# Optimization experiments

Measured on AMD Instinct MI355X. Metric: run time of the kernel, lower is better.

The kernel has to match this reference:

```python
import jax, jax.numpy as jnp
import numpy as np

B, T, N_EMBD = 1, 2048, 2048
N_HEAD = 16
KV_LOW = 512      # kv_low_rank == head_size (compressed value dim)
Q_LOW = 1024
ROPE_HS = 64
QK_HS = KV_LOW + ROPE_HS  # 576
HEAD_SIZE = KV_LOW        # v_equiv = c_kv.view(B,1,T,head_size)


def _rope_tables(seq_len, dim, base=10000.0):
    # litgpt-style: theta over half dim, duplicated to full dim
    inv = 1.0 / (base ** (np.arange(0, dim, 2, dtype=np.float32) / dim))
    t = np.arange(seq_len, dtype=np.float32)
    freqs = np.outer(t, inv)                      # [T, dim/2]
    emb = np.concatenate([freqs, freqs], axis=-1)  # [T, dim]
    return jnp.asarray(np.cos(emb)), jnp.asarray(np.sin(emb))


def _apply_rope(x, cos, sin):
    # x: [..., T, d]; cos/sin broadcastable [T, d]. rotate-half RoPE.
    d = x.shape[-1]
    x1, x2 = x[..., : d // 2], x[..., d // 2:]
    rotated = jnp.concatenate([-x2, x1], axis=-1)
    return x * cos + rotated * sin


def setup_inputs() -> dict:
    key = jax.random.key(0)
    ks = jax.random.split(key, 4)
    x = jax.random.normal(ks[0], (B, T, N_EMBD), dtype=jnp.float32)
    cos, sin = _rope_tables(T, ROPE_HS)
    s = 0.02
    W_qkv = jax.random.normal(ks[1], (N_EMBD, KV_LOW + ROPE_HS + Q_LOW), dtype=jnp.float32) * s
    W_qdec = jax.random.normal(ks[2], (Q_LOW, N_HEAD * QK_HS), dtype=jnp.float32) * s
    W_out = jax.random.normal(ks[3], (N_HEAD * HEAD_SIZE, N_EMBD), dtype=jnp.float32) * s
    return {"x": x, "cos": cos, "sin": sin, "W_qkv": W_qkv, "W_qdec": W_qdec, "W_out": W_out}


def reference(x, cos, sin, W_qkv, W_qdec, W_out):
    Bq, Tq, _ = x.shape
    # latent encoding and split
    latents = x @ W_qkv                                       # [B,T,kv+rope+q]
    c_kv = latents[..., :KV_LOW]                              # [B,T,512] (keys-nope and values)
    k_r = latents[..., KV_LOW:KV_LOW + ROPE_HS]               # [B,T,64]
    c_q = latents[..., KV_LOW + ROPE_HS:]                     # [B,T,1024]
    # per-head query decode
    q = (c_q @ W_qdec).reshape(Bq, Tq, N_HEAD, QK_HS)         # [B,T,H,576]
    q_nope, q_r = q[..., :KV_LOW], q[..., KV_LOW:]
    # partial RoPE
    k_r = _apply_rope(k_r, cos, sin)                          # [B,T,64]
    q_r = _apply_rope(q_r, cos[None, :, None, :], sin[None, :, None, :])  # [B,T,H,64]
    q = jnp.concatenate([q_nope, q_r], axis=-1)               # [B,T,H,576]
    q = jnp.swapaxes(q, 1, 2)                                 # [B,H,T,576]
    k = jnp.concatenate([c_kv, k_r], axis=-1)                 # [B,T,576] shared across heads
    v = c_kv                                                  # [B,T,512] shared across heads
    scale = 1.0 / jnp.sqrt(jnp.float32(HEAD_SIZE))
    scores = jnp.einsum('bhtd,bsd->bhts', q, k) * scale       # [B,H,T,T]
    causal = jnp.tril(jnp.ones((Tq, Tq), dtype=bool))
    scores = jnp.where(causal, scores, jnp.finfo(scores.dtype).min)
    attn = jax.nn.softmax(scores, axis=-1)
    y = jnp.einsum('bhts,bsd->bhtd', attn, v)                 # [B,H,T,512]
    y = jnp.swapaxes(y, 1, 2).reshape(Bq, Tq, N_HEAD * HEAD_SIZE)
    return y @ W_out                                          # [B,T,n_embd]
```

## Files before the change

kernel.cpp:

```cpp
#include <hip/hip_runtime.h>

typedef __bf16 bf16x8_t __attribute__((ext_vector_type(8)));
typedef float f32x4_t __attribute__((ext_vector_type(4)));

#define LAT_LD 1664
#define QK_DIM 576
#define V_DIM 512
#define NHEAD 16
#define TSEQ 2048
#define QLD 9216
#define YLD 8192
#define KLD 576
#define SCALE 0.044194173824159216f

__device__ __forceinline__ unsigned short f2bf(float f) {
  union { float f; unsigned int u; } v; v.f = f;
  unsigned int r = v.u + 0x7FFFu + ((v.u >> 16) & 1u);
  return (unsigned short)(r >> 16);
}

__device__ __forceinline__ void load_lds16(const unsigned short* g, unsigned short* l) {
  __builtin_amdgcn_global_load_lds((const __attribute__((address_space(1))) void*)g,
                                   (__attribute__((address_space(3))) void*)l, 16, 0, 0);
}

__device__ __forceinline__ void conv_t_body(const float* __restrict__ src, int R, int Csrc,
                                            unsigned short* __restrict__ dst,
                                            int bx, int by, int tid,
                                            unsigned short (*T)[72]) {
  const int r0 = bx * 64, c0 = by * 64;
  const bool live = (c0 < Csrc);
#pragma unroll
  for (int it = 0; it < 4; ++it) {
    int idx = it * 256 + tid;
    int r = idx >> 4, c4 = (idx & 15) * 4;
    float4 v = {0.f, 0.f, 0.f, 0.f};
    if (live) v = *(const float4*)&src[(size_t)(r0 + r) * Csrc + c0 + c4];
    T[c4 + 0][r] = f2bf(v.x);
    T[c4 + 1][r] = f2bf(v.y);
    T[c4 + 2][r] = f2bf(v.z);
    T[c4 + 3][r] = f2bf(v.w);
  }
  __syncthreads();
#pragma unroll
  for (int it = 0; it < 2; ++it) {
    int idx = it * 256 + tid;
    int cc = idx >> 3, r8 = (idx & 7) * 8;
    uint4 v = *(const uint4*)&T[cc][r8];
    *(uint4*)&dst[(size_t)(c0 + cc) * R + r0 + r8] = v;
  }
}

__global__ __launch_bounds__(256) void prep_all(
    const float* __restrict__ x, unsigned short* __restrict__ xb,
    const float* __restrict__ wqkv, unsigned short* __restrict__ wqkvT,
    const float* __restrict__ wqdec, unsigned short* __restrict__ wqdecT,
    const float* __restrict__ wout, unsigned short* __restrict__ woutT,
    float* __restrict__ lsum) {
  __shared__ unsigned short T[64][72];
  const int blk = blockIdx.x, tid = threadIdx.x;
  if (blk < 4096) {
    int i = (blk * 256 + tid) * 4;
    float4 v = *(const float4*)&x[i];
    ushort4 o;
    o.x = f2bf(v.x); o.y = f2bf(v.y); o.z = f2bf(v.z); o.w = f2bf(v.w);
    *(ushort4*)&xb[i] = o;
  } else if (blk < 4928) {
    int l = blk - 4096;
    conv_t_body(wqkv, 2048, 1600, wqkvT, l & 31, l >> 5, tid, T);
  } else if (blk < 7232) {
    int l = blk - 4928;
    conv_t_body(wqdec, 1024, 9216, wqdecT, l & 15, l >> 4, tid, T);
  } else if (blk < 11328) {
    int l = blk - 7232;
    conv_t_body(wout, 8192, 2048, woutT, l & 127, l >> 7, tid, T);
  } else {
    int i = ((blk - 11328) * 256 + tid) * 4;
    *(float4*)&lsum[i] = (float4){0.f, 0.f, 0.f, 0.f};
  }
}

__global__ __launch_bounds__(256) void postlat(
    const float* __restrict__ P1,
    unsigned short* __restrict__ lat,
    unsigned short* __restrict__ kbuf,
    unsigned short* __restrict__ vtg,
    const float* __restrict__ cosb, const float* __restrict__ sinb) {
  __shared__ unsigned short T[64][72];
  const int tid = threadIdx.x;
  const int bx = blockIdx.x, by = blockIdx.y;
  const int r0 = bx * 64, c0 = by * 64;
  const size_t n = (size_t)2048 * 1664;

#pragma unroll
  for (int it = 0; it < 4; ++it) {
    int idx = it * 256 + tid;
    int r = idx >> 4, c4 = (idx & 15) * 4;
    size_t off = (size_t)(r0 + r) * 1664 + c0 + c4;
    float4 a = *(const float4*)&P1[off];
    float4 b = *(const float4*)&P1[n + off];
    ushort4 o;
    o.x = f2bf(a.x + b.x); o.y = f2bf(a.y + b.y);
    o.z = f2bf(a.z + b.z); o.w = f2bf(a.w + b.w);
    if (by < 8) {
      *(ushort4*)&kbuf[(size_t)(r0 + r) * KLD + c0 + c4] = o;
      T[c4 + 0][r] = o.x; T[c4 + 1][r] = o.y; T[c4 + 2][r] = o.z; T[c4 + 3][r] = o.w;
    } else if (by == 8) {
      T[r][c4 + 0] = o.x; T[r][c4 + 1] = o.y; T[r][c4 + 2] = o.z; T[r][c4 + 3] = o.w;
    } else {
      *(ushort4*)&lat[(size_t)(r0 + r) * LAT_LD + c0 + c4] = o;
    }
  }
  if (by > 8) return;
  __syncthreads();
  if (by < 8) {
#pragma unroll
    for (int it = 0; it < 2; ++it) {
      int idx = it * 256 + tid;
      int cc = idx >> 3, r8 = (idx & 7) * 8;
      uint4 v = *(const uint4*)&T[cc][r8];
      *(uint4*)&vtg[(size_t)(c0 + cc) * TSEQ + r0 + r8] = v;
    }
  } else {
#pragma unroll
    for (int it = 0; it < 8; ++it) {
      int idx = it * 256 + tid;
      int r = idx >> 5, d = idx & 31;
      int t = r0 + r;
      union { unsigned int u; float f; } a, b;
      a.u = ((unsigned int)T[r][d]) << 16;
      b.u = ((unsigned int)T[r][d + 32]) << 16;
      float c0f = cosb[t * 64 + d], s0f = sinb[t * 64 + d];
      float c1f = cosb[t * 64 + d + 32], s1f = sinb[t * 64 + d + 32];
      kbuf[(size_t)t * KLD + 512 + d] = f2bf(a.f * c0f - b.f * s0f);
      kbuf[(size_t)t * KLD + 544 + d] = f2bf(b.f * c1f + a.f * s1f);
    }
  }
}

#define GEMM_PROLOGUE()                                                     \
  __shared__ __align__(16) unsigned short As[8192];                         \
  __shared__ __align__(16) unsigned short Bs[8192];                         \
  const int tid = threadIdx.x;                                              \
  const int wave = tid >> 6, lane = tid & 63;                               \
  const int quad = lane >> 4, l16 = lane & 15;                              \
  const int wm = wave >> 1, wn = wave & 1;                                  \
  f32x4_t acc[4][4];                                                        \
  f32x4_t zero = {0.f, 0.f, 0.f, 0.f};                                      \
  _Pragma("unroll") for (int mi = 0; mi < 4; ++mi)                          \
    _Pragma("unroll") for (int ni = 0; ni < 4; ++ni) acc[mi][ni] = zero;

#define GEMM_KLOOP(Aptr, Alda, Bptr, Bldb, M0, N0, KLEN)                    \
  for (int k0 = 0; k0 < (KLEN); k0 += 64) {                                 \
    _Pragma("unroll") for (int p2 = 0; p2 < 2; ++p2) {                      \
      int ci = p2 * 256 + tid;                                              \
      int rr2 = ci >> 2, cc2 = (ci & 3) * 8;                                \
      const unsigned short* ga = &(Aptr)[(size_t)((M0) + rr2) * (Alda) + k0 + cc2]; \
      const unsigned short* gb = &(Bptr)[(size_t)((N0) + rr2) * (Bldb) + k0 + cc2]; \
      load_lds16(ga,      &As[ci * 8]);                                     \
      load_lds16(ga + 32, &As[4096 + ci * 8]);                              \
      load_lds16(gb,      &Bs[ci * 8]);                                     \
      load_lds16(gb + 32, &Bs[4096 + ci * 8]);                              \
    }                                                                       \
    __syncthreads();                                                        \
    _Pragma("unroll") for (int hf = 0; hf < 2; ++hf) {                      \
      bf16x8_t af[4], bfr[4];                                               \
      _Pragma("unroll") for (int mi = 0; mi < 4; ++mi)                      \
        af[mi] = *(const bf16x8_t*)&As[hf * 4096 + (wm * 64 + mi * 16 + l16) * 32 + quad * 8]; \
      _Pragma("unroll") for (int ni = 0; ni < 4; ++ni)                      \
        bfr[ni] = *(const bf16x8_t*)&Bs[hf * 4096 + (wn * 64 + ni * 16 + l16) * 32 + quad * 8]; \
      _Pragma("unroll") for (int mi = 0; mi < 4; ++mi)                      \
        _Pragma("unroll") for (int ni = 0; ni < 4; ++ni)                    \
          acc[mi][ni] = __builtin_amdgcn_mfma_f32_16x16x32_bf16(af[mi], bfr[ni], acc[mi][ni], 0, 0, 0); \
    }                                                                       \
    __syncthreads();                                                        \
  }

__global__ __launch_bounds__(256, 2) void gemm_splitk(
    const unsigned short* __restrict__ A, int lda,
    const unsigned short* __restrict__ Bt, int ldb,
    float* __restrict__ P, int ldc, int Ks) {
  const int m0 = blockIdx.y * 128, n0 = blockIdx.x * 128;
  const size_t koff = (size_t)blockIdx.z * Ks;
  const unsigned short* Ap = A + koff;
  const unsigned short* Bp = Bt + koff;
  float* C = P + (size_t)blockIdx.z * ((size_t)gridDim.y * 128) * ldc;
  GEMM_PROLOGUE();
  GEMM_KLOOP(Ap, lda, Bp, ldb, m0, n0, Ks);
#pragma unroll
  for (int mi = 0; mi < 4; ++mi)
#pragma unroll
    for (int ni = 0; ni < 4; ++ni)
#pragma unroll
      for (int r = 0; r < 4; ++r) {
        int row = m0 + wm * 64 + mi * 16 + quad * 4 + r;
        int col = n0 + wn * 64 + ni * 16 + l16;
        C[(size_t)row * ldc + col] = acc[mi][ni][r];
      }
}

__global__ __launch_bounds__(256, 2) void gemm_qdec(
    const unsigned short* __restrict__ A,
    const unsigned short* __restrict__ Bt,
    unsigned short* __restrict__ qbuf,
    const float* __restrict__ cosb, const float* __restrict__ sinb) {
  const int m0 = blockIdx.y * 128, n0 = blockIdx.x * 128;
  GEMM_PROLOGUE();
  GEMM_KLOOP(A, LAT_LD, Bt, 1024, m0, n0, 1024);

  const int cb = n0 + wn * 64;
  const bool ropeh = (cb % QK_DIM) == 512;
#pragma unroll
  for (int mi = 0; mi < 4; ++mi)
#pragma unroll
    for (int r = 0; r < 4; ++r) {
      int t = m0 + wm * 64 + mi * 16 + quad * 4 + r;
      if (ropeh) {
#pragma unroll
        for (int ni = 0; ni < 2; ++ni) {
          int d = ni * 16 + l16;
          float c0f = cosb[t * 64 + d], s0f = sinb[t * 64 + d];
          float c1f = cosb[t * 64 + d + 32], s1f = sinb[t * 64 + d + 32];
          float v1 = acc[mi][ni][r], v2 = acc[mi][ni + 2][r];
          qbuf[(size_t)t * QLD + cb + d] = f2bf(v1 * c0f - v2 * s0f);
          qbuf[(size_t)t * QLD + cb + 32 + d] = f2bf(v2 * c1f + v1 * s1f);
        }
      } else {
#pragma unroll
        for (int ni = 0; ni < 4; ++ni)
          qbuf[(size_t)t * QLD + cb + ni * 16 + l16] = f2bf(acc[mi][ni][r]);
      }
    }
}

__global__ __launch_bounds__(256) void reduce4_f32(const float* __restrict__ p,
                                                   float* __restrict__ dst, int n) {
  int i = (blockIdx.x * 256 + threadIdx.x) * 4;
  if (i < n) {
    float4 a = *(const float4*)&p[i];
    float4 b = *(const float4*)&p[(size_t)n + i];
    float4 c = *(const float4*)&p[2 * (size_t)n + i];
    float4 d = *(const float4*)&p[3 * (size_t)n + i];
    float4 o;
    o.x = (a.x + b.x) + (c.x + d.x);
    o.y = (a.y + b.y) + (c.y + d.y);
    o.z = (a.z + b.z) + (c.z + d.z);
    o.w = (a.w + b.w) + (c.w + d.w);
    *(float4*)&dst[i] = o;
  }
}

__global__ __launch_bounds__(256, 2) void qke_kernel(
    const unsigned short* __restrict__ qbuf,
    const unsigned short* __restrict__ kbuf,
    unsigned short* __restrict__ Ebuf,
    float* __restrict__ lsum, int hbase) {
  int tx = blockIdx.x, ig = 15, cnt = 16;
  while (tx >= cnt) { tx -= cnt; --ig; --cnt; }
  const int j = tx;
  const int hl = blockIdx.y, h = hbase + hl;
  const int Kmax = (ig + 1) << 7;
  const int r0g = ig << 7;
  const int pre = (ig * (ig + 1)) >> 1;

  const unsigned short* A = qbuf + (size_t)r0g * QLD + h * QK_DIM;
  const unsigned short* Bt = kbuf + (size_t)(j << 7) * KLD;
  unsigned short* Eh = Ebuf + ((size_t)hl * 136 + pre) * 16384;

  GEMM_PROLOGUE();
  GEMM_KLOOP(A, QLD, Bt, KLD, 0, 0, QK_DIM);

#pragma unroll
  for (int mi = 0; mi < 4; ++mi) {
    float rs[4] = {0.f, 0.f, 0.f, 0.f};
#pragma unroll
    for (int ni = 0; ni < 4; ++ni)
#pragma unroll
      for (int r = 0; r < 4; ++r) {
        int qr = r0g + wm * 64 + mi * 16 + quad * 4 + r;
        int key = (j << 7) + wn * 64 + ni * 16 + l16;
        float e = (key <= qr) ? __expf(acc[mi][ni][r] * SCALE) : 0.f;
        rs[r] += e;
        Eh[(size_t)(qr - r0g) * Kmax + key] = f2bf(e);
      }
#pragma unroll
    for (int r = 0; r < 4; ++r) {
      float s = rs[r];
#pragma unroll
      for (int off = 1; off < 16; off <<= 1) s += __shfl_xor(s, off, 64);
      if (l16 == 0) {
        int qr = r0g + wm * 64 + mi * 16 + quad * 4 + r;
        atomicAdd(&lsum[h * TSEQ + qr], s);
      }
    }
  }
}

__global__ __launch_bounds__(256, 2) void pv_kernel(
    const unsigned short* __restrict__ Ebuf,
    const unsigned short* __restrict__ vtg,
    const float* __restrict__ lsum,
    unsigned short* __restrict__ ybuf, int hbase) {
  const int ig = 15 - blockIdx.y;
  const int hl = blockIdx.z, h = hbase + hl;
  const int n0 = blockIdx.x * 128;
  const int Kmax = (ig + 1) << 7;
  const int pre = (ig * (ig + 1)) >> 1;

  const unsigned short* A = Ebuf + ((size_t)hl * 136 + pre) * 16384;

  GEMM_PROLOGUE();
  GEMM_KLOOP(A, Kmax, vtg, TSEQ, 0, n0, Kmax);

#pragma unroll
  for (int mi = 0; mi < 4; ++mi)
#pragma unroll
    for (int r = 0; r < 4; ++r) {
      int row_g = (ig << 7) + wm * 64 + mi * 16 + quad * 4 + r;
      float inv = 1.f / lsum[h * TSEQ + row_g];
#pragma unroll
      for (int ni = 0; ni < 4; ++ni) {
        int col = h * V_DIM + n0 + wn * 64 + ni * 16 + l16;
        ybuf[(size_t)row_g * YLD + col] = f2bf(acc[mi][ni][r] * inv);
      }
    }
}

extern "C" void kernel_launch(void* const* d_in, const int* in_sizes, int n_in,
                              void* d_out, int out_size, void* d_ws, size_t ws_size,
                              hipStream_t stream) {
  (void)in_sizes; (void)n_in; (void)out_size; (void)ws_size;
  const float* x     = (const float*)d_in[0];
  const float* cosb  = (const float*)d_in[1];
  const float* sinb  = (const float*)d_in[2];
  const float* wqkv  = (const float*)d_in[3];
  const float* wqdec = (const float*)d_in[4];
  const float* wout  = (const float*)d_in[5];
  float* out = (float*)d_out;

  unsigned short* ws     = (unsigned short*)d_ws;
  unsigned short* xb     = ws;
  unsigned short* wqkvT  = xb     + (size_t)2048 * 2048;
  unsigned short* wqdecT = wqkvT  + (size_t)1664 * 2048;
  unsigned short* lat    = wqdecT + (size_t)9216 * 1024;
  unsigned short* qbuf   = lat    + (size_t)2048 * 1664;
  unsigned short* woutT  = qbuf   + (size_t)2048 * 9216;
  unsigned short* ybuf   = woutT  + (size_t)2048 * 8192;
  unsigned short* vtg    = ybuf   + (size_t)2048 * 8192;
  unsigned short* kbuf   = vtg    + (size_t)512 * 2048;
  float*          lsumf  = (float*)(kbuf + (size_t)2048 * 576);
  unsigned short* Ebuf   = ws;
  float*          P1     = (float*)qbuf;
  float*          Pf     = (float*)ws;

  prep_all<<<11360, 256, 0, stream>>>(x, xb, wqkv, wqkvT, wqdec, wqdecT, wout, woutT, lsumf);

  gemm_splitk<<<dim3(13, 16, 2), 256, 0, stream>>>(xb, 2048, wqkvT, 2048, P1, 1664, 1024);
  postlat<<<dim3(32, 26), 256, 0, stream>>>(P1, lat, kbuf, vtg, cosb, sinb);

  gemm_qdec<<<dim3(72, 16), 256, 0, stream>>>(lat + 576, wqdecT, qbuf, cosb, sinb);

  qke_kernel<<<dim3(136, 8), 256, 0, stream>>>(qbuf, kbuf, Ebuf, lsumf, 0);
  pv_kernel<<<dim3(4, 16, 8), 256, 0, stream>>>(Ebuf, vtg, lsumf, ybuf, 0);
  qke_kernel<<<dim3(136, 8), 256, 0, stream>>>(qbuf, kbuf, Ebuf, lsumf, 8);
  pv_kernel<<<dim3(4, 16, 8), 256, 0, stream>>>(Ebuf, vtg, lsumf, ybuf, 8);

  gemm_splitk<<<dim3(16, 16, 4), 256, 0, stream>>>(ybuf, YLD, woutT, 8192, Pf, 2048, 2048);
  reduce4_f32<<<4096, 256, 0, stream>>>(Pf, out, 2048 * 2048);
}
```

Before: 498.3 us.

## Use 256x256 tiled GEMM with interleaved staging for qdec and output projection

Adds a 512-thread, 256x256-tile GEMM main loop that double-buffers 64-wide K slices in LDS. It uses an XOR-swizzled layout and splits each K step into four MFMA phases, with async global-to-LDS loads issued between them. The query-decode GEMM (with fused RoPE epilogue) and the output-projection split-K GEMM now use it, and qdec also remaps block indices for L2 locality. Larger tiles raise arithmetic intensity and cut redundant operand loads, at the cost of fewer blocks (288 and 256), which may underfill the CUs, and heavier register pressure.

```diff
diff --git a/kernel.cpp b/kernel.cpp
--- a/kernel.cpp
+++ b/kernel.cpp
@@ -199,31 +199,167 @@
       }
 }
 
-__global__ __launch_bounds__(256, 2) void gemm_qdec(
+#define SWZ(o) ((o) ^ ((((o) >> 9) & 1) << 5))
+#define SBAR() do { __builtin_amdgcn_s_barrier(); __builtin_amdgcn_sched_barrier(0); } while (0)
+#define VMCNT(n) asm volatile("s_waitcnt vmcnt(" #n ")" ::: "memory")
+
+__device__ __forceinline__ bf16x8_t frag_ld256(const unsigned short* region, int rl, int kk, int quad) {
+  int lin = rl * 128 + kk * 64 + quad * 16;
+  lin ^= ((rl >> 2) & 1) << 5;
+  return *(const bf16x8_t*)((const unsigned char*)region + lin);
+}
+
+__device__ __forceinline__ void stage256(
+    const unsigned short* __restrict__ A, int lda, int m0,
+    const unsigned short* __restrict__ Bt, int ldb, int n0,
+    unsigned short* lds, int s, int NT4,
+    int srow0, int scol0, int srow1, int scol1, int tid) {
+  if (s >= NT4) return;
+  const int u = s >> 2, kind = s & 3;
+  unsigned short* dst = lds + ((u & 1) << 15) + (kind << 13);
+  const unsigned short* gb = (kind < 2) ? A : Bt;
+  const int ld = (kind < 2) ? lda : ldb;
+  const int rb = ((kind < 2) ? m0 : n0) + (kind & 1) * 128;
+  const int c0 = u * 64;
+  load_lds16(gb + (size_t)(rb + srow0) * ld + c0 + scol0, dst + tid * 8);
+  load_lds16(gb + (size_t)(rb + srow1) * ld + c0 + scol1, dst + 4096 + tid * 8);
+}
+
+#define MFMA16(MB, BREG, NB)                                                \
+  __builtin_amdgcn_s_setprio(1);                                            \
+  _Pragma("unroll") for (int mi = 0; mi < 4; ++mi)                          \
+    _Pragma("unroll") for (int ni = 0; ni < 2; ++ni)                        \
+      _Pragma("unroll") for (int kk = 0; kk < 2; ++kk)                      \
+        acc[(MB) + mi][(NB) + ni] = __builtin_amdgcn_mfma_f32_16x16x32_bf16( \
+            a[(MB) + mi][kk], BREG[ni][kk], acc[(MB) + mi][(NB) + ni], 0, 0, 0); \
+  __builtin_amdgcn_s_setprio(0);
+
+__device__ __forceinline__ void kloop256(
+    const unsigned short* __restrict__ A, int lda, int m0,
+    const unsigned short* __restrict__ Bt, int ldb, int n0,
+    int NT, unsigned short* lds, f32x4_t (&acc)[8][4],
+    int tid, int quad, int l16, int wm, int wn) {
+  const int NT4 = NT << 2;
+  const int o0 = tid * 16, o1 = 8192 + tid * 16;
+  const int so0 = SWZ(o0), so1 = SWZ(o1);
+  const int srow0 = so0 >> 7, scol0 = (so0 & 127) >> 1;
+  const int srow1 = so1 >> 7, scol1 = (so1 & 127) >> 1;
+  auto STG = [&](int s) {
+    stage256(A, lda, m0, Bt, ldb, n0, lds, s, NT4, srow0, scol0, srow1, scol1, tid);
+  };
+  STG(0); STG(1); STG(2); STG(3);
+  VMCNT(4);
+  STG(4); STG(5); STG(6);
+  VMCNT(6);
+  SBAR();
+  const int brow = (wn & 1) * 64;
+  for (int t = 0; t < NT; ++t) {
+    const unsigned short* Ar = lds + ((t & 1) << 15) + (wm << 13);
+    const unsigned short* Br = lds + ((t & 1) << 15) + 16384 + ((wn >> 1) << 13);
+    bf16x8_t a[8][2], b0[2][2], b1[2][2];
+#pragma unroll
+    for (int mi = 0; mi < 8; ++mi) {
+      a[mi][0] = frag_ld256(Ar, mi * 16 + l16, 0, quad);
+      a[mi][1] = frag_ld256(Ar, mi * 16 + l16, 1, quad);
+    }
+#pragma unroll
+    for (int ni = 0; ni < 2; ++ni) {
+      b0[ni][0] = frag_ld256(Br, brow + ni * 16 + l16, 0, quad);
+      b0[ni][1] = frag_ld256(Br, brow + ni * 16 + l16, 1, quad);
+    }
+    STG(4 * t + 7);
+    SBAR();
+    MFMA16(0, b0, 0);
+    SBAR();
+#pragma unroll
+    for (int ni = 0; ni < 2; ++ni) {
+      b1[ni][0] = frag_ld256(Br, brow + (2 + ni) * 16 + l16, 0, quad);
+      b1[ni][1] = frag_ld256(Br, brow + (2 + ni) * 16 + l16, 1, quad);
+    }
+    STG(4 * t + 8);
+    SBAR();
+    MFMA16(0, b1, 2);
+    SBAR();
+    STG(4 * t + 9);
+    SBAR();
+    MFMA16(4, b1, 2);
+    SBAR();
+    STG(4 * t + 10);
+    SBAR();
+    MFMA16(4, b0, 0);
+    if (t < NT - 2) { VMCNT(6); }
+    else if (t == NT - 2) { VMCNT(0); }
+    SBAR();
+  }
+}
+
+__global__ __launch_bounds__(512, 2) void gemm256_splitk(
+    const unsigned short* __restrict__ A, int lda,
+    const unsigned short* __restrict__ Bt, int ldb,
+    float* __restrict__ P, int ldc, int Ks) {
+  __shared__ __align__(16) unsigned short lds[65536];
+  const int tid = threadIdx.x;
+  const int quad = (tid >> 4) & 3, l16 = tid & 15;
+  const int wave = tid >> 6, wm = wave >> 2, wn = wave & 3;
+  const int m0 = blockIdx.y * 256, n0 = blockIdx.x * 256;
+  const unsigned short* Ap = A + (size_t)blockIdx.z * Ks;
+  const unsigned short* Bp = Bt + (size_t)blockIdx.z * Ks;
+  float* C = P + (size_t)blockIdx.z * ((size_t)gridDim.y * 256) * ldc;
+  f32x4_t acc[8][4];
+  f32x4_t z4 = {0.f, 0.f, 0.f, 0.f};
+#pragma unroll
+  for (int mi = 0; mi < 8; ++mi)
+#pragma unroll
+    for (int ni = 0; ni < 4; ++ni) acc[mi][ni] = z4;
+  kloop256(Ap, lda, m0, Bp, ldb, n0, Ks >> 6, lds, acc, tid, quad, l16, wm, wn);
+#pragma unroll
+  for (int mi = 0; mi < 8; ++mi)
+#pragma unroll
+    for (int ni = 0; ni < 4; ++ni)
+#pragma unroll
+      for (int r = 0; r < 4; ++r) {
+        const int row = m0 + wm * 128 + mi * 16 + quad * 4 + r;
+        const int col = n0 + wn * 64 + ni * 16 + l16;
+        C[(size_t)row * ldc + col] = acc[mi][ni][r];
+      }
+}
+
+__global__ __launch_bounds__(512, 2) void gemm256_qdec(
     const unsigned short* __restrict__ A,
     const unsigned short* __restrict__ Bt,
     unsigned short* __restrict__ qbuf,
     const float* __restrict__ cosb, const float* __restrict__ sinb) {
-  const int m0 = blockIdx.y * 128, n0 = blockIdx.x * 128;
-  GEMM_PROLOGUE();
-  GEMM_KLOOP(A, LAT_LD, Bt, 1024, m0, n0, 1024);
+  __shared__ __align__(16) unsigned short lds[65536];
+  const int tid = threadIdx.x;
+  const int quad = (tid >> 4) & 3, l16 = tid & 15;
+  const int wave = tid >> 6, wm = wave >> 2, wn = wave & 3;
+  const int d = blockIdx.y * gridDim.x + blockIdx.x;
+  const int wg = (d & 7) * 36 + (d >> 3);
+  const int m0 = (wg / 36) * 256, n0 = (wg % 36) * 256;
+  f32x4_t acc[8][4];
+  f32x4_t z4 = {0.f, 0.f, 0.f, 0.f};
+#pragma unroll
+  for (int mi = 0; mi < 8; ++mi)
+#pragma unroll
+    for (int ni = 0; ni < 4; ++ni) acc[mi][ni] = z4;
+  kloop256(A, LAT_LD, m0, Bt, 1024, n0, 16, lds, acc, tid, quad, l16, wm, wn);
 
   const int cb = n0 + wn * 64;
   const bool ropeh = (cb % QK_DIM) == 512;
 #pragma unroll
-  for (int mi = 0; mi < 4; ++mi)
+  for (int mi = 0; mi < 8; ++mi)
 #pragma unroll
     for (int r = 0; r < 4; ++r) {
-      int t = m0 + wm * 64 + mi * 16 + quad * 4 + r;
+      const int t = m0 + wm * 128 + mi * 16 + quad * 4 + r;
       if (ropeh) {
 #pragma unroll
         for (int ni = 0; ni < 2; ++ni) {
-          int d = ni * 16 + l16;
-          float c0f = cosb[t * 64 + d], s0f = sinb[t * 64 + d];
-          float c1f = cosb[t * 64 + d + 32], s1f = sinb[t * 64 + d + 32];
+          const int dd = ni * 16 + l16;
+          float c0f = cosb[t * 64 + dd], s0f = sinb[t * 64 + dd];
+          float c1f = cosb[t * 64 + dd + 32], s1f = sinb[t * 64 + dd + 32];
           float v1 = acc[mi][ni][r], v2 = acc[mi][ni + 2][r];
-          qbuf[(size_t)t * QLD + cb + d] = f2bf(v1 * c0f - v2 * s0f);
-          qbuf[(size_t)t * QLD + cb + 32 + d] = f2bf(v2 * c1f + v1 * s1f);
+          qbuf[(size_t)t * QLD + cb + dd] = f2bf(v1 * c0f - v2 * s0f);
+          qbuf[(size_t)t * QLD + cb + 32 + dd] = f2bf(v2 * c1f + v1 * s1f);
         }
       } else {
 #pragma unroll
@@ -358,13 +494,13 @@
   gemm_splitk<<<dim3(13, 16, 2), 256, 0, stream>>>(xb, 2048, wqkvT, 2048, P1, 1664, 1024);
   postlat<<<dim3(32, 26), 256, 0, stream>>>(P1, lat, kbuf, vtg, cosb, sinb);
 
-  gemm_qdec<<<dim3(72, 16), 256, 0, stream>>>(lat + 576, wqdecT, qbuf, cosb, sinb);
+  gemm256_qdec<<<dim3(36, 8), 512, 0, stream>>>(lat + 576, wqdecT, qbuf, cosb, sinb);
 
   qke_kernel<<<dim3(136, 8), 256, 0, stream>>>(qbuf, kbuf, Ebuf, lsumf, 0);
   pv_kernel<<<dim3(4, 16, 8), 256, 0, stream>>>(Ebuf, vtg, lsumf, ybuf, 0);
   qke_kernel<<<dim3(136, 8), 256, 0, stream>>>(qbuf, kbuf, Ebuf, lsumf, 8);
   pv_kernel<<<dim3(4, 16, 8), 256, 0, stream>>>(Ebuf, vtg, lsumf, ybuf, 8);
 
-  gemm_splitk<<<dim3(16, 16, 4), 256, 0, stream>>>(ybuf, YLD, woutT, 8192, Pf, 2048, 2048);
+  gemm256_splitk<<<dim3(8, 8, 4), 512, 0, stream>>>(ybuf, 8192, woutT, 8192, Pf, 2048, 2048);
   reduce4_f32<<<4096, 256, 0, stream>>>(Pf, out, 2048 * 2048);
 }
```

Result: slower. 657.0 us (+31.8%).
